# Kernel optimization log

Hardware: AMD Instinct MI355X
Metric: run time of the kernel (lower is better)

## Reference

```python
import jax, jax.numpy as jnp
import numpy as np

N_NODES = 50000
N_EDGES = 800000
IN_F = 128
OUT_F = 128
N_LAYERS = 2


def setup_inputs() -> dict:
    key = jax.random.key(0)
    ks = jax.random.split(key, 8)
    x = jax.random.normal(ks[0], (N_NODES, IN_F), dtype=jnp.float32)
    hidden_states = jax.random.normal(ks[1], (N_LAYERS, N_NODES, OUT_F), dtype=jnp.float32)
    src = jax.random.randint(ks[2], (N_EDGES,), 0, N_NODES)
    dst = jax.random.randint(ks[3], (N_EDGES,), 0, N_NODES)
    edge_w = jax.random.uniform(ks[4], (N_EDGES,), dtype=jnp.float32)
    # [layer, gate(r,u,c), in+out, out], scaled like typical init
    W_self = jax.random.normal(ks[5], (N_LAYERS, 3, IN_F + OUT_F, OUT_F), dtype=jnp.float32) * 0.05
    W_neigh = jax.random.normal(ks[6], (N_LAYERS, 3, IN_F + OUT_F, OUT_F), dtype=jnp.float32) * 0.05
    bias = jax.random.uniform(ks[7], (N_LAYERS, 3, OUT_F), dtype=jnp.float32)
    return {"x": x, "hidden_states": hidden_states, "src": src, "dst": dst,
            "edge_w": edge_w, "W_self": W_self, "W_neigh": W_neigh, "bias": bias}


def _gconv(z, src, dst, edge_w, ws, wn):
    # z: [N, 2F]; message passing: sum_{e: dst=v} edge_w[e] * z[src[e]]
    msg = z[src] * edge_w[:, None]                      # [E, 2F]
    agg = jax.ops.segment_sum(msg, dst, num_segments=N_NODES)  # [N, 2F]
    return z @ ws + agg @ wn                            # [N, F]


def _cell(x, h, src, dst, edge_w, ws, wn, b):
    # ws/wn: [3, 2F, F], b: [3, F]; gates r,u,c as in GraphGRUCell
    xh = jnp.concatenate([x, h], axis=1)
    r = jax.nn.sigmoid(_gconv(xh, src, dst, edge_w, ws[0], wn[0]) + b[0])
    u = jax.nn.sigmoid(_gconv(xh, src, dst, edge_w, ws[1], wn[1]) + b[1])
    xh2 = jnp.concatenate([x, r * h], axis=1)
    c = jax.nn.sigmoid(_gconv(xh2, src, dst, edge_w, ws[2], wn[2]) + b[2])
    return u * h + (1.0 - u) * c


def reference(x, hidden_states, src, dst, edge_w, W_self, W_neigh, bias):
    hiddens = []
    for i in range(N_LAYERS):  # small fixed layer count
        x = _cell(x, hidden_states[i], src, dst, edge_w, W_self[i], W_neigh[i], bias[i])
        hiddens.append(x)
    return (x, hiddens)
```

## Files before the change

kernel.cpp:

```cpp
#include <hip/hip_runtime.h>
#include <math.h>

#define F 128
#define NLAYERS 2

typedef __attribute__((ext_vector_type(8))) short bf16x8s;
typedef __attribute__((ext_vector_type(4))) float f32x4;

__device__ __forceinline__ float sigmoidf_(float x) { return 1.0f / (1.0f + expf(-x)); }

__device__ __forceinline__ unsigned short f2bf(float f) {
    unsigned int u = __float_as_uint(f);
    u += 0x7fffu + ((u >> 16) & 1u);
    return (unsigned short)(u >> 16);
}
__device__ __forceinline__ float bf2f(unsigned short s) {
    return __uint_as_float(((unsigned int)s) << 16);
}

__global__ void pack_w_bf16(const float* __restrict__ Ws, const float* __restrict__ Wn,
                            unsigned short* __restrict__ W1b, unsigned short* __restrict__ W2b) {
    int t = blockIdx.x * blockDim.x + threadIdx.x;
    const int n1 = 2 * 64 * 256 * 8;
    if (t < n1) {
        int j = t & 7, n = (t >> 3) & 255, ko = (t >> 11) & 63, l = t >> 17;
        int k = ko * 8 + j;
        int p = k >> 7, r = k & 127, g = n >> 7, c = n & 127;
        const float* W = (p < 2) ? Ws : Wn;
        W1b[t] = f2bf(W[(((l * 3 + g) * 256) + ((p & 1) * 128 + r)) * 128 + c]);
    } else {
        int t2 = t - n1;
        if (t2 >= 2 * 64 * 128 * 8) return;
        int j = t2 & 7, n = (t2 >> 3) & 127, ko = (t2 >> 10) & 63, l = t2 >> 16;
        int k = ko * 8 + j;
        int p = k >> 7, r = k & 127;
        const float* W = (p < 2) ? Ws : Wn;
        W2b[t2] = f2bf(W[(((l * 3 + 2) * 256) + ((p & 1) * 128 + r)) * 128 + n]);
    }
}

__global__ void cvt_bf16(const float* __restrict__ in, unsigned short* __restrict__ out, int n4) {
    int t = blockIdx.x * blockDim.x + threadIdx.x;
    if (t >= n4) return;
    float4 v = reinterpret_cast<const float4*>(in)[t];
    ushort4 o;
    o.x = f2bf(v.x); o.y = f2bf(v.y); o.z = f2bf(v.z); o.w = f2bf(v.w);
    reinterpret_cast<ushort4*>(out)[t] = o;
}

__global__ void hist_dst(const int* __restrict__ dst, int* __restrict__ cnt, int E) {
    int e = blockIdx.x * blockDim.x + threadIdx.x;
    if (e < E) atomicAdd(&cnt[dst[e]], 1);
}

__global__ __launch_bounds__(1024) void scan_offs(const int* __restrict__ cnt,
                                                  int* __restrict__ offs,
                                                  int* __restrict__ cursor, int n) {
    __shared__ int wsum[16];
    __shared__ int carry_s;
    int tid = threadIdx.x;
    int lane = tid & 63, wid = tid >> 6;
    if (tid == 0) carry_s = 0;
    __syncthreads();
    for (int base = 0; base < n; base += 1024) {
        int i = base + tid;
        int v = (i < n) ? cnt[i] : 0;
        int incl = v;
#pragma unroll
        for (int off = 1; off < 64; off <<= 1) {
            int t = __shfl_up(incl, off, 64);
            if (lane >= off) incl += t;
        }
        if (lane == 63) wsum[wid] = incl;
        __syncthreads();
        if (wid == 0) {
            int s = (lane < 16) ? wsum[lane] : 0;
#pragma unroll
            for (int off = 1; off < 16; off <<= 1) {
                int t = __shfl_up(s, off, 64);
                if (lane >= off) s += t;
            }
            if (lane < 16) wsum[lane] = s;
        }
        __syncthreads();
        int wbase = (wid > 0) ? wsum[wid - 1] : 0;
        int carry = carry_s;
        int excl = carry + wbase + incl - v;
        if (i < n) { offs[i] = excl; cursor[i] = excl; }
        __syncthreads();
        if (tid == 1023) carry_s = carry + wsum[15];
        __syncthreads();
    }
    if (threadIdx.x == 0) offs[n] = carry_s;
}

__global__ void scatter_edges(const int* __restrict__ src, const int* __restrict__ dst,
                              const float* __restrict__ ew, int* __restrict__ cursor,
                              int2* __restrict__ es, int E) {
    int e = blockIdx.x * blockDim.x + threadIdx.x;
    if (e >= E) return;
    int d = dst[e];
    int p = atomicAdd(&cursor[d], 1);
    es[p] = make_int2(src[e], __float_as_int(ew[e]));
}

__global__ __launch_bounds__(256) void agg_csr2_b(
    const unsigned short* __restrict__ V0, const unsigned short* __restrict__ V1,
    const int2* __restrict__ es, const int* __restrict__ offs,
    unsigned short* __restrict__ agg0, unsigned short* __restrict__ agg1, int N) {
    int node = blockIdx.x * 8 + (threadIdx.x >> 5);
    if (node >= N) return;
    int lane = threadIdx.x & 31;
    int beg = offs[node], end = offs[node + 1];
    float p0[4] = {0, 0, 0, 0}, q0[4] = {0, 0, 0, 0};
    float p1[4] = {0, 0, 0, 0}, q1[4] = {0, 0, 0, 0};
    int i = beg;
    for (; i + 1 < end; i += 2) {
        int2 e0 = es[i], e1 = es[i + 1];
        float w0 = __int_as_float(e0.y), w1 = __int_as_float(e1.y);
        size_t r0 = ((size_t)e0.x << 7) + (lane << 2);
        size_t r1 = ((size_t)e1.x << 7) + (lane << 2);
        ushort4 x0 = *reinterpret_cast<const ushort4*>(V0 + r0);
        ushort4 x1 = *reinterpret_cast<const ushort4*>(V0 + r1);
        ushort4 h0 = *reinterpret_cast<const ushort4*>(V1 + r0);
        ushort4 h1 = *reinterpret_cast<const ushort4*>(V1 + r1);
        p0[0] += w0 * bf2f(x0.x); p0[1] += w0 * bf2f(x0.y);
        p0[2] += w0 * bf2f(x0.z); p0[3] += w0 * bf2f(x0.w);
        p1[0] += w1 * bf2f(x1.x); p1[1] += w1 * bf2f(x1.y);
        p1[2] += w1 * bf2f(x1.z); p1[3] += w1 * bf2f(x1.w);
        q0[0] += w0 * bf2f(h0.x); q0[1] += w0 * bf2f(h0.y);
        q0[2] += w0 * bf2f(h0.z); q0[3] += w0 * bf2f(h0.w);
        q1[0] += w1 * bf2f(h1.x); q1[1] += w1 * bf2f(h1.y);
        q1[2] += w1 * bf2f(h1.z); q1[3] += w1 * bf2f(h1.w);
    }
    if (i < end) {
        int2 e0 = es[i];
        float w0 = __int_as_float(e0.y);
        size_t r0 = ((size_t)e0.x << 7) + (lane << 2);
        ushort4 x0 = *reinterpret_cast<const ushort4*>(V0 + r0);
        ushort4 h0 = *reinterpret_cast<const ushort4*>(V1 + r0);
        p0[0] += w0 * bf2f(x0.x); p0[1] += w0 * bf2f(x0.y);
        p0[2] += w0 * bf2f(x0.z); p0[3] += w0 * bf2f(x0.w);
        q0[0] += w0 * bf2f(h0.x); q0[1] += w0 * bf2f(h0.y);
        q0[2] += w0 * bf2f(h0.z); q0[3] += w0 * bf2f(h0.w);
    }
    size_t ob = ((size_t)node << 7) + (lane << 2);
    ushort4 o0, o1;
    o0.x = f2bf(p0[0] + p1[0]); o0.y = f2bf(p0[1] + p1[1]);
    o0.z = f2bf(p0[2] + p1[2]); o0.w = f2bf(p0[3] + p1[3]);
    o1.x = f2bf(q0[0] + q1[0]); o1.y = f2bf(q0[1] + q1[1]);
    o1.z = f2bf(q0[2] + q1[2]); o1.w = f2bf(q0[3] + q1[3]);
    *reinterpret_cast<ushort4*>(agg0 + ob) = o0;
    *reinterpret_cast<ushort4*>(agg1 + ob) = o1;
}

__global__ __launch_bounds__(256) void agg_csr1_b(
    const unsigned short* __restrict__ V0,
    const int2* __restrict__ es, const int* __restrict__ offs,
    unsigned short* __restrict__ agg0, int N) {
    int node = blockIdx.x * 8 + (threadIdx.x >> 5);
    if (node >= N) return;
    int lane = threadIdx.x & 31;
    int beg = offs[node], end = offs[node + 1];
    float p0[4] = {0, 0, 0, 0}, p1[4] = {0, 0, 0, 0};
    int i = beg;
    for (; i + 1 < end; i += 2) {
        int2 e0 = es[i], e1 = es[i + 1];
        float w0 = __int_as_float(e0.y), w1 = __int_as_float(e1.y);
        size_t r0 = ((size_t)e0.x << 7) + (lane << 2);
        size_t r1 = ((size_t)e1.x << 7) + (lane << 2);
        ushort4 x0 = *reinterpret_cast<const ushort4*>(V0 + r0);
        ushort4 x1 = *reinterpret_cast<const ushort4*>(V0 + r1);
        p0[0] += w0 * bf2f(x0.x); p0[1] += w0 * bf2f(x0.y);
        p0[2] += w0 * bf2f(x0.z); p0[3] += w0 * bf2f(x0.w);
        p1[0] += w1 * bf2f(x1.x); p1[1] += w1 * bf2f(x1.y);
        p1[2] += w1 * bf2f(x1.z); p1[3] += w1 * bf2f(x1.w);
    }
    if (i < end) {
        int2 e0 = es[i];
        float w0 = __int_as_float(e0.y);
        size_t r0 = ((size_t)e0.x << 7) + (lane << 2);
        ushort4 x0 = *reinterpret_cast<const ushort4*>(V0 + r0);
        p0[0] += w0 * bf2f(x0.x); p0[1] += w0 * bf2f(x0.y);
        p0[2] += w0 * bf2f(x0.z); p0[3] += w0 * bf2f(x0.w);
    }
    size_t ob = ((size_t)node << 7) + (lane << 2);
    ushort4 o0;
    o0.x = f2bf(p0[0] + p1[0]); o0.y = f2bf(p0[1] + p1[1]);
    o0.z = f2bf(p0[2] + p1[2]); o0.w = f2bf(p0[3] + p1[3]);
    *reinterpret_cast<ushort4*>(agg0 + ob) = o0;
}

__global__ __launch_bounds__(256) void gemm_mfma(
    const unsigned short* __restrict__ A0, const unsigned short* __restrict__ A1,
    const unsigned short* __restrict__ A2, const unsigned short* __restrict__ A3,
    const unsigned short* __restrict__ Wb, const float* __restrict__ bias,
    const float* __restrict__ hfull, const float* __restrict__ uin,
    unsigned short* __restrict__ outb, float* __restrict__ outf,
    float* __restrict__ outf2, int Nn, int Ntot, int mode) {
    __shared__ __align__(16) unsigned short Als[2][4 * 64 * 8];
    __shared__ __align__(16) unsigned short Bls[2][4 * 128 * 8];
    const unsigned short* parts[4] = {A0, A1, A2, A3};

    int tid = threadIdx.x;
    int row0 = blockIdx.x * 64;
    int n0c = blockIdx.y * 128;
    int lane = tid & 63;
    int w = tid >> 6;
    int wrow = (w & 1) << 5;
    int wcol = (w >> 1) << 6;
    int quad = lane >> 4, l16 = lane & 15;

    f32x4 acc[2][4];
    const f32x4 z4 = {0.f, 0.f, 0.f, 0.f};
#pragma unroll
    for (int mt = 0; mt < 2; ++mt)
#pragma unroll
        for (int nt = 0; nt < 4; ++nt) acc[mt][nt] = z4;

    int growA = row0 + lane;
    if (growA >= Nn) growA = Nn - 1;
    int qB = tid >> 7, nB = tid & 127;

    auto stage = [&](int ks, int buf) {
        const unsigned short* ga = parts[ks >> 7] + ((size_t)growA << 7) + (ks & 127) + (w << 3);
        __builtin_amdgcn_global_load_lds(
            (const __attribute__((address_space(1))) void*)ga,
            (__attribute__((address_space(3))) void*)&Als[buf][((w << 6) + lane) << 3], 16, 0, 0);
#pragma unroll
        for (int r = 0; r < 2; ++r) {
            int q = 2 * r + qB;
            int koG = (ks >> 3) + q;
            const unsigned short* gb = Wb + ((size_t)(koG * Ntot + n0c + nB) << 3);
            __builtin_amdgcn_global_load_lds(
                (const __attribute__((address_space(1))) void*)gb,
                (__attribute__((address_space(3))) void*)&Bls[buf][((q << 7) + nB) << 3], 16, 0, 0);
        }
    };

    stage(0, 0);
    __syncthreads();
    int buf = 0;
    for (int ks = 0; ks < 512; ks += 32, buf ^= 1) {
        if (ks + 32 < 512) stage(ks + 32, buf ^ 1);

        bf16x8s af[2], bfr[4];
#pragma unroll
        for (int mt = 0; mt < 2; ++mt)
            af[mt] = *reinterpret_cast<const bf16x8s*>(
                &Als[buf][((quad << 6) + wrow + (mt << 4) + l16) << 3]);
#pragma unroll
        for (int nt = 0; nt < 4; ++nt)
            bfr[nt] = *reinterpret_cast<const bf16x8s*>(
                &Bls[buf][((quad << 7) + wcol + (nt << 4) + l16) << 3]);
#pragma unroll
        for (int mt = 0; mt < 2; ++mt)
#pragma unroll
            for (int nt = 0; nt < 4; ++nt)
                acc[mt][nt] = __builtin_amdgcn_mfma_f32_16x16x32_bf16(
                    af[mt], bfr[nt], acc[mt][nt], 0, 0, 0);
        __syncthreads();
    }

#pragma unroll
    for (int mt = 0; mt < 2; ++mt) {
#pragma unroll
        for (int reg = 0; reg < 4; ++reg) {
            int row = row0 + wrow + (mt << 4) + (quad << 2) + reg;
            if (row >= Nn) continue;
#pragma unroll
            for (int nt = 0; nt < 4; ++nt) {
                int col = n0c + wcol + (nt << 4) + l16;
                float val = acc[mt][nt][reg] + bias[col];
                if (mode == 0) {
                    float sg = sigmoidf_(val);
                    int c = col & 127;
                    size_t o = ((size_t)row << 7) + c;
                    if (col < 128)
                        outb[o] = f2bf(sg * hfull[o]);
                    else
                        outf[o] = sg;
                } else {
                    float cv = sigmoidf_(val);
                    size_t o = ((size_t)row << 7) + col;
                    float uu = uin[o];
                    float hh = hfull[o];
                    float hn = uu * hh + (1.0f - uu) * cv;
                    outf[o] = hn;
                    if (outf2) outf2[o] = hn;
                    outb[o] = f2bf(hn);
                }
            }
        }
    }
}

extern "C" void kernel_launch(void* const* d_in, const int* in_sizes, int n_in,
                              void* d_out, int out_size, void* d_ws, size_t ws_size,
                              hipStream_t stream) {
    const float* x      = (const float*)d_in[0];
    const float* hidden = (const float*)d_in[1];
    const int*   src    = (const int*)d_in[2];
    const int*   dst    = (const int*)d_in[3];
    const float* ew     = (const float*)d_in[4];
    const float* Wself  = (const float*)d_in[5];
    const float* Wneigh = (const float*)d_in[6];
    const float* bias   = (const float*)d_in[7];
    float* out = (float*)d_out;

    int N = in_sizes[0] / F;
    int E = in_sizes[2];
    size_t NF = (size_t)N * F;

    char* p = (char*)d_ws;
    auto alloc = [&](size_t bytes) { char* r = p; p += (bytes + 255) & ~255ull; return r; };
    unsigned short* xb0    = (unsigned short*)alloc(NF * 2);
    unsigned short* xb1    = (unsigned short*)alloc(NF * 2);
    unsigned short* hb     = (unsigned short*)alloc(2 * NF * 2);
    unsigned short* agg_xb = (unsigned short*)alloc(NF * 2);
    unsigned short* agg_hb = (unsigned short*)alloc(NF * 2);
    unsigned short* agg_rb = (unsigned short*)alloc(NF * 2);
    unsigned short* rhb    = (unsigned short*)alloc(NF * 2);
    float*          u      = (float*)alloc(NF * 4);
    unsigned short* W1b    = (unsigned short*)alloc(2 * 64 * 256 * 8 * 2);
    unsigned short* W2b    = (unsigned short*)alloc(2 * 64 * 128 * 8 * 2);
    int2*           es     = (int2*)alloc((size_t)E * 8);
    int*            cnt    = (int*)alloc((size_t)N * 4);
    int*            offs   = (int*)alloc(((size_t)N + 1) * 4);
    int*            cursor = (int*)alloc((size_t)N * 4);

    pack_w_bf16<<<dim3(1536), dim3(256), 0, stream>>>(Wself, Wneigh, W1b, W2b);
    cvt_bf16<<<dim3((int)(NF / 4 + 255) / 256, 1), dim3(256), 0, stream>>>(x, xb0, (int)(NF / 4));
    cvt_bf16<<<dim3((int)(2 * NF / 4 + 255) / 256, 1), dim3(256), 0, stream>>>(hidden, hb, (int)(2 * NF / 4));

    hipMemsetAsync(cnt, 0, (size_t)N * sizeof(int), stream);
    int eBlocks = (E + 255) / 256;
    hist_dst<<<dim3(eBlocks), dim3(256), 0, stream>>>(dst, cnt, E);
    scan_offs<<<dim3(1), dim3(1024), 0, stream>>>(cnt, offs, cursor, N);
    scatter_edges<<<dim3(eBlocks), dim3(256), 0, stream>>>(src, dst, ew, cursor, es, E);

    float* out_x  = out;
    float* out_h1 = out + NF;
    float* out_h2 = out + 2 * NF;

    int aggBlocks = (N + 7) / 8;
    int mBlocks = (N + 63) / 64;
    for (int l = 0; l < NLAYERS; ++l) {
        const unsigned short* xbL = (l == 0) ? xb0 : xb1;
        const unsigned short* hbL = hb + (size_t)l * NF;
        const float* hL = hidden + (size_t)l * NF;
        const float* biasL = bias + (size_t)l * 384;

        agg_csr2_b<<<dim3(aggBlocks), dim3(256), 0, stream>>>(xbL, hbL, es, offs,
                                                              agg_xb, agg_hb, N);

        gemm_mfma<<<dim3(mBlocks, 2), dim3(256), 0, stream>>>(
            xbL, hbL, agg_xb, agg_hb,
            W1b + (size_t)l * 64 * 256 * 8, biasL, hL, nullptr,
            rhb, u, nullptr, N, 256, 0);

        agg_csr1_b<<<dim3(aggBlocks), dim3(256), 0, stream>>>(rhb, es, offs, agg_rb, N);

        float* o1 = (l == 0) ? out_h1 : out_h2;
        float* o2 = (l == NLAYERS - 1) ? out_x : nullptr;
        unsigned short* xbN = (l == 0) ? xb1 : xb0;
        gemm_mfma<<<dim3(mBlocks, 1), dim3(256), 0, stream>>>(
            xbL, rhb, agg_xb, agg_rb,
            W2b + (size_t)l * 64 * 128 * 8, biasL + 256, hL, u,
            xbN, o1, o2, N, 128, 1);
    }
}
```

Baseline: 664.1 us.

## Load GEMM operands directly from global into registers with larger row tiles

Removes the LDS double-buffered staging in the MFMA GEMM. Each wave now loads its A and B fragments straight from global memory into registers, and the K loop is fully unrolled with no barriers. The block tile grows from 64 to 128 rows (4x4 MFMA tiles per wave), which halves the number of row blocks and doubles the reuse of B fragments per wave. The trade-off is that A/B data is no longer shared between waves through LDS, so each wave issues more global/L2 traffic, and register pressure goes up.

```diff
diff --git a/kernel.cpp b/kernel.cpp
--- a/kernel.cpp
+++ b/kernel.cpp
@@ -198,72 +198,56 @@
     const float* __restrict__ hfull, const float* __restrict__ uin,
     unsigned short* __restrict__ outb, float* __restrict__ outf,
     float* __restrict__ outf2, int Nn, int Ntot, int mode) {
-    __shared__ __align__(16) unsigned short Als[2][4 * 64 * 8];
-    __shared__ __align__(16) unsigned short Bls[2][4 * 128 * 8];
     const unsigned short* parts[4] = {A0, A1, A2, A3};
 
     int tid = threadIdx.x;
-    int row0 = blockIdx.x * 64;
+    int row0 = blockIdx.x * 128;
     int n0c = blockIdx.y * 128;
     int lane = tid & 63;
     int w = tid >> 6;
-    int wrow = (w & 1) << 5;
+    int wrow = (w & 1) << 6;
     int wcol = (w >> 1) << 6;
     int quad = lane >> 4, l16 = lane & 15;
 
-    f32x4 acc[2][4];
+    int rowA[4];
+#pragma unroll
+    for (int mt = 0; mt < 4; ++mt) {
+        int r = row0 + wrow + (mt << 4) + l16;
+        rowA[mt] = (r < Nn) ? r : (Nn - 1);
+    }
+    int colB[4];
+#pragma unroll
+    for (int nt = 0; nt < 4; ++nt) colB[nt] = n0c + wcol + (nt << 4) + l16;
+
+    f32x4 acc[4][4];
     const f32x4 z4 = {0.f, 0.f, 0.f, 0.f};
 #pragma unroll
-    for (int mt = 0; mt < 2; ++mt)
+    for (int mt = 0; mt < 4; ++mt)
 #pragma unroll
         for (int nt = 0; nt < 4; ++nt) acc[mt][nt] = z4;
 
-    int growA = row0 + lane;
-    if (growA >= Nn) growA = Nn - 1;
-    int qB = tid >> 7, nB = tid & 127;
-
-    auto stage = [&](int ks, int buf) {
-        const unsigned short* ga = parts[ks >> 7] + ((size_t)growA << 7) + (ks & 127) + (w << 3);
-        __builtin_amdgcn_global_load_lds(
-            (const __attribute__((address_space(1))) void*)ga,
-            (__attribute__((address_space(3))) void*)&Als[buf][((w << 6) + lane) << 3], 16, 0, 0);
-#pragma unroll
-        for (int r = 0; r < 2; ++r) {
-            int q = 2 * r + qB;
-            int koG = (ks >> 3) + q;
-            const unsigned short* gb = Wb + ((size_t)(koG * Ntot + n0c + nB) << 3);
-            __builtin_amdgcn_global_load_lds(
-                (const __attribute__((address_space(1))) void*)gb,
-                (__attribute__((address_space(3))) void*)&Bls[buf][((q << 7) + nB) << 3], 16, 0, 0);
-        }
-    };
-
-    stage(0, 0);
-    __syncthreads();
-    int buf = 0;
-    for (int ks = 0; ks < 512; ks += 32, buf ^= 1) {
-        if (ks + 32 < 512) stage(ks + 32, buf ^ 1);
-
-        bf16x8s af[2], bfr[4];
-#pragma unroll
-        for (int mt = 0; mt < 2; ++mt)
-            af[mt] = *reinterpret_cast<const bf16x8s*>(
-                &Als[buf][((quad << 6) + wrow + (mt << 4) + l16) << 3]);
+#pragma unroll
+    for (int ks = 0; ks < 512; ks += 32) {
+        const unsigned short* Ap = parts[ks >> 7];
+        int cb = (ks & 127) + (quad << 3);
+        int koG = (ks >> 3) + quad;
+        bf16x8s af[4], bfr[4];
+#pragma unroll
+        for (int mt = 0; mt < 4; ++mt)
+            af[mt] = *reinterpret_cast<const bf16x8s*>(Ap + (((size_t)rowA[mt]) << 7) + cb);
 #pragma unroll
         for (int nt = 0; nt < 4; ++nt)
-            bfr[nt] = *reinterpret_cast<const bf16x8s*>(
-                &Bls[buf][((quad << 7) + wcol + (nt << 4) + l16) << 3]);
-#pragma unroll
-        for (int mt = 0; mt < 2; ++mt)
+            bfr[nt] = *reinterpret_cast<const bf16x8s*>(Wb + (((size_t)(koG * Ntot + colB[nt])) << 3));
+#pragma unroll
+        for (int mt = 0; mt < 4; ++mt)
 #pragma unroll
             for (int nt = 0; nt < 4; ++nt)
                 acc[mt][nt] = __builtin_amdgcn_mfma_f32_16x16x32_bf16(
                     af[mt], bfr[nt], acc[mt][nt], 0, 0, 0);
-        __syncthreads();
-    }
-
-#pragma unroll
-    for (int mt = 0; mt < 2; ++mt) {
+    }
+
+#pragma unroll
+    for (int mt = 0; mt < 4; ++mt) {
 #pragma unroll
         for (int reg = 0; reg < 4; ++reg) {
             int row = row0 + wrow + (mt << 4) + (quad << 2) + reg;
@@ -344,7 +328,7 @@
     float* out_h2 = out + 2 * NF;
 
     int aggBlocks = (N + 7) / 8;
-    int mBlocks = (N + 63) / 64;
+    int mBlocks = (N + 127) / 128;
     for (int l = 0; l < NLAYERS; ++l) {
         const unsigned short* xbL = (l == 0) ? xb0 : xb1;
         const unsigned short* hbL = hb + (size_t)l * NF;
```

New measurement: 740.5 us. 11.5% more time.
